# Kernel optimization log

Measured on AMD Instinct MI355X. Metric: run time of the kernel, lower is better.

The kernel has to match this reference:

```python
import jax, jax.numpy as jnp
import numpy as np

BS = 8            # self.b from __init__
NSAMPLE = 32      # self.nsample
EPS_TCR = 0.2     # TotalCodingRate eps
COS_EPS = 1e-8    # torch cosine_similarity eps


def setup_inputs() -> dict:
    key = jax.random.key(0)
    k0, k1, k2, k3, k4 = jax.random.split(key, 5)
    B, N, C = 8, 8192, 64
    return {
        "logits": jax.random.normal(k0, (B, N, C), jnp.float32),
        "logits1": jax.random.normal(k1, (B, N, C), jnp.float32),
        "p0first": jax.random.uniform(k2, (B, N, 3), jnp.float32),
        "p0sec": jax.random.uniform(k3, (B, N, 3), jnp.float32),
        "orixyz": jax.random.uniform(k4, (B, N, 3), jnp.float32),
    }


def _fps(p, m):
    # furthest point sampling, seed = point 0; p: [b,n,3] -> idx [b,m] int32
    b, n, _ = p.shape
    batch = jnp.arange(b)
    d0 = jnp.sum((p - p[:, :1]) ** 2, -1)  # [b,n] sq dist to seed

    def step(dist, _):
        nxt = jnp.argmax(dist, axis=1)                 # [b]
        pn = p[batch, nxt]                             # [b,3]
        dist = jnp.minimum(dist, jnp.sum((p - pn[:, None]) ** 2, -1))
        return dist, nxt

    _, idxs = jax.lax.scan(step, d0, None, length=m - 1)  # [m-1,b]
    return jnp.concatenate(
        [jnp.zeros((b, 1), jnp.int32), idxs.T.astype(jnp.int32)], axis=1)


def _knn_idx(q, s, k):
    # q: [b,m,3] queries, s: [b,n,3] support -> [b,m,k] neighbor indices
    d = (jnp.sum(q * q, -1)[:, :, None] + jnp.sum(s * s, -1)[:, None, :]
         - 2.0 * jnp.einsum('bmd,bnd->bmn', q, s))
    _, idx = jax.lax.top_k(-d, k)  # smallest distances
    return idx


def _group_losses(fi, fj, c):
    # fi: [b,m,c] center feats, fj: [b,m,k,c] neighbor feats
    # per group: datatemp = cat(fj, fi) -> [K=k+1, c]
    D = jnp.concatenate([fj, fi[:, :, None, :]], axis=2)  # [b,m,K,c]
    avg = D.mean(axis=2, keepdims=True)                   # [b,m,1,c]
    num = jnp.sum(D * avg, -1)                            # [b,m,K]
    den = jnp.maximum(
        jnp.linalg.norm(D, axis=-1) * jnp.linalg.norm(avg, axis=-1), COS_EPS)
    loss_contract = -(num / den).mean(axis=2)             # [b,m] (Similarity_Loss)
    # TotalCodingRate on each single row z: -0.5*logdet(I + (c/(BS*eps)) z z^T)
    #   = -0.5*log(1 + (c/(BS*eps)) ||z||^2)   (rank-1 identity)
    scalar = c / (BS * EPS_TCR)
    loss_tcr = (-0.5 * jnp.log1p(scalar * jnp.sum(D * D, -1))).mean(axis=2)
    return jnp.sum(200.0 * loss_contract + 1.0 * loss_tcr, axis=1)  # [b]


def reference(logits, logits1, p0first, p0sec, orixyz):
    b, n, c = logits.shape
    ds = n // 16  # downsample

    # global per-point cosine loss
    num = jnp.sum(logits * logits1, -1)
    den = jnp.maximum(
        jnp.linalg.norm(logits, axis=-1) * jnp.linalg.norm(logits1, axis=-1),
        COS_EPS)
    globalpointloss = -jnp.mean(num / den)

    idx = _fps(p0first, ds)   # [b,ds]
    idx1 = _fps(p0sec, ds)
    new_p = jnp.take_along_axis(p0first, idx[..., None], axis=1)   # [b,ds,3]
    new_p1 = jnp.take_along_axis(p0sec, idx1[..., None], axis=1)
    fi = jnp.take_along_axis(logits, idx[..., None], axis=1)       # [b,ds,c]
    fi1 = jnp.take_along_axis(logits1, idx1[..., None], axis=1)

    ki = _knn_idx(new_p, p0first, NSAMPLE)    # [b,ds,k]
    ki1 = _knn_idx(new_p1, p0sec, NSAMPLE)
    fj = jax.vmap(lambda f, i: f[i])(logits, ki)    # [b,ds,k,c]
    fj1 = jax.vmap(lambda f, i: f[i])(logits1, ki1)

    # per-batch summed group-inner losses (both views)
    S = _group_losses(fi, fj, c) + _group_losses(fi1, fj1, c)  # [b]

    # faithful to original: running total divided by downsample each batch iter
    def fold(g, s):
        return (g + s) / ds, None
    groupinnerloss, _ = jax.lax.scan(fold, jnp.float32(0.0), S)
    groupinnerloss = groupinnerloss / b

    # original returns globalpointloss + groupinnerloss + groupinnerloss
    # (groupouterloss is computed but never used in the returned loss)
    return globalpointloss + groupinnerloss + groupinnerloss
```

## Files before the change

### kernel.cpp

```cpp
#include <hip/hip_runtime.h>
#include <cstdint>

#define NPTS 8192
#define NB 8
#define DS 512
#define CF 64
#define KNN 32
#define NFPS 16
#define NWORK 240
#define NCOSI 64
#define NITEMS (NCOSI + 2 * NB * DS)
#define DYNLDS 98304

typedef float v2f __attribute__((ext_vector_type(2)));
typedef unsigned long long ull;

__device__ __forceinline__ float wave_max63(float x) {
  int v;
  v = __builtin_amdgcn_update_dpp(0, __float_as_int(x), 0x111, 0xf, 0xf, true); x = fmaxf(x, __int_as_float(v));
  v = __builtin_amdgcn_update_dpp(0, __float_as_int(x), 0x112, 0xf, 0xf, true); x = fmaxf(x, __int_as_float(v));
  v = __builtin_amdgcn_update_dpp(0, __float_as_int(x), 0x114, 0xf, 0xf, true); x = fmaxf(x, __int_as_float(v));
  v = __builtin_amdgcn_update_dpp(0, __float_as_int(x), 0x118, 0xf, 0xf, true); x = fmaxf(x, __int_as_float(v));
  v = __builtin_amdgcn_update_dpp(0, __float_as_int(x), 0x142, 0xf, 0xf, true); x = fmaxf(x, __int_as_float(v));
  v = __builtin_amdgcn_update_dpp(0, __float_as_int(x), 0x143, 0xf, 0xf, true); x = fmaxf(x, __int_as_float(v));
  return x;
}

__device__ __forceinline__ float wave_sum_bcast(float x) {
  int v;
  v = __builtin_amdgcn_update_dpp(0, __float_as_int(x), 0x111, 0xf, 0xf, true); x += __int_as_float(v);
  v = __builtin_amdgcn_update_dpp(0, __float_as_int(x), 0x112, 0xf, 0xf, true); x += __int_as_float(v);
  v = __builtin_amdgcn_update_dpp(0, __float_as_int(x), 0x114, 0xf, 0xf, true); x += __int_as_float(v);
  v = __builtin_amdgcn_update_dpp(0, __float_as_int(x), 0x118, 0xf, 0xf, true); x += __int_as_float(v);
  v = __builtin_amdgcn_update_dpp(0, __float_as_int(x), 0x142, 0xf, 0xf, true); x += __int_as_float(v);
  v = __builtin_amdgcn_update_dpp(0, __float_as_int(x), 0x143, 0xf, 0xf, true); x += __int_as_float(v);
  return __int_as_float(__builtin_amdgcn_readlane(__float_as_int(x), 63));
}

__global__ __launch_bounds__(64) void zero_kernel(float* __restrict__ acc) {
  if (threadIdx.x < 16) acc[threadIdx.x] = 0.0f;
}

__global__ __launch_bounds__(512, 2) void fused_kernel(
    const float* __restrict__ logits, const float* __restrict__ logits1,
    const float* __restrict__ p0first, const float* __restrict__ p0sec,
    int* __restrict__ idxbuf, float* __restrict__ acc,
    int* __restrict__ done, float* __restrict__ out) {
  extern __shared__ char smem[];
  __shared__ __align__(16) ull wslot[2][4];
  __shared__ int wtot[8];
  __shared__ int s_bl[2];
  __shared__ int ctr, eqctr, s_center;
  __shared__ float wloss[8];

  const int blk = blockIdx.x;
  const int t = threadIdx.x;

  if (blk < NFPS) {
    float* ldsP = (float*)smem;
    const int view = blk >> 3, b = blk & 7;
    const float* p = (view ? p0sec : p0first) + (size_t)b * NPTS * 3;
    int* idx_out = idxbuf + blk * DS;
    const int lane = t & 63, wave = t >> 6;

    if (t < 256) {
      v2f px2[16], py2[16], pz2[16], dist2[16];
      {
        const float4* p4 = (const float4*)p;
        float4* l4 = (float4*)ldsP;
#pragma unroll
        for (int k = 0; k < 8; ++k) {
          float4 v0 = p4[t * 24 + 3 * k + 0];
          float4 v1 = p4[t * 24 + 3 * k + 1];
          float4 v2 = p4[t * 24 + 3 * k + 2];
          l4[t * 24 + 3 * k + 0] = v0;
          l4[t * 24 + 3 * k + 1] = v1;
          l4[t * 24 + 3 * k + 2] = v2;
          px2[2 * k]     = (v2f){v0.x, v0.w};
          py2[2 * k]     = (v2f){v0.y, v1.x};
          pz2[2 * k]     = (v2f){v0.z, v1.y};
          px2[2 * k + 1] = (v2f){v1.z, v2.y};
          py2[2 * k + 1] = (v2f){v1.w, v2.z};
          pz2[2 * k + 1] = (v2f){v2.x, v2.w};
          dist2[2 * k] = (v2f){3.4e38f, 3.4e38f};
          dist2[2 * k + 1] = (v2f){3.4e38f, 3.4e38f};
        }
      }
#pragma unroll
      for (int g = 0; g < 16; ++g) {
        asm("" : "+v"(px2[g]), "+v"(py2[g]), "+v"(pz2[g]));
      }
      if (t == 0)
        __hip_atomic_store(&idx_out[0], 0, __ATOMIC_RELAXED, __HIP_MEMORY_SCOPE_AGENT);
      float wx = p[0], wy = p[1], wz = p[2];
      __syncthreads();

      for (int it = 0; it < DS - 1; ++it) {
        v2f wx2 = (v2f){wx, wx}, wy2 = (v2f){wy, wy}, wz2 = (v2f){wz, wz};
#pragma unroll
        for (int g = 0; g < 16; ++g) {
          v2f dx = px2[g] - wx2, dy = py2[g] - wy2, dz = pz2[g] - wz2;
          v2f nd = dx * dx + dy * dy + dz * dz;
          dist2[g] = __builtin_elementwise_min(dist2[g], nd);
        }
        v2f m0 = __builtin_elementwise_max(dist2[0], dist2[1]);
        v2f m1 = __builtin_elementwise_max(dist2[2], dist2[3]);
        v2f m2 = __builtin_elementwise_max(dist2[4], dist2[5]);
        v2f m3 = __builtin_elementwise_max(dist2[6], dist2[7]);
        v2f m4 = __builtin_elementwise_max(dist2[8], dist2[9]);
        v2f m5 = __builtin_elementwise_max(dist2[10], dist2[11]);
        v2f m6 = __builtin_elementwise_max(dist2[12], dist2[13]);
        v2f m7 = __builtin_elementwise_max(dist2[14], dist2[15]);
        v2f n0 = __builtin_elementwise_max(m0, m1);
        v2f n1 = __builtin_elementwise_max(m2, m3);
        v2f n2 = __builtin_elementwise_max(m4, m5);
        v2f n3 = __builtin_elementwise_max(m6, m7);
        v2f o0 = __builtin_elementwise_max(n0, n1);
        v2f o1 = __builtin_elementwise_max(n2, n3);
        v2f q = __builtin_elementwise_max(o0, o1);
        float lm = fmaxf(q.x, q.y);
        float wmv = wave_max63(lm);
        float wm = __int_as_float(__builtin_amdgcn_readlane(__float_as_int(wmv), 63));
        ull cmask = __ballot(lm == wm);
        int winlane = (int)__ffsll(cmask) - 1;
        if (lane == winlane) {
          int jbest = 0;
#pragma unroll
          for (int jp = 31; jp >= 0; --jp) {
            float dv = (jp & 1) ? dist2[jp >> 1].y : dist2[jp >> 1].x;
            if (dv == lm) jbest = jp;
          }
          unsigned e_best = ((unsigned)t << 5) | (unsigned)jbest;
          wslot[it & 1][wave] =
              (((ull)__float_as_uint(wm)) << 32) | (ull)(8191u - e_best);
        }
        asm volatile("s_waitcnt lgkmcnt(0)\n\ts_barrier" ::: "memory");
        {
          const ull* ws = wslot[it & 1];
          ull k0 = ws[0], k1 = ws[1], k2 = ws[2], k3 = ws[3];
          ull a0 = k0 > k1 ? k0 : k1, a1 = k2 > k3 ? k2 : k3;
          ull kb = a0 > a1 ? a0 : a1;
          unsigned e = 8191u - (unsigned)(kb & 0xffffffffu);
          if (t == 0)
            __hip_atomic_store(&idx_out[it + 1], (int)e, __ATOMIC_RELAXED,
                               __HIP_MEMORY_SCOPE_AGENT);
          wx = ldsP[e * 3 + 0]; wy = ldsP[e * 3 + 1]; wz = ldsP[e * 3 + 2];
        }
      }
    } else {
      __syncthreads();
      for (int it = 0; it < DS - 1; ++it)
        asm volatile("s_waitcnt lgkmcnt(0)\n\ts_barrier" ::: "memory");
    }
  } else {
    int* hb0 = (int*)smem;
    int* hb1 = (int*)(smem + 16384);
    float* Drows = (float*)(smem + 32768);
    int* nbr = (int*)(smem + 41216);
    int* eq = (int*)(smem + 41344);
    const int lane = t & 63, wave = t >> 6;
    const int w0 = blk - NFPS;
    for (int item = w0; item < NITEMS; item += NWORK) {
      if (item < NCOSI) {
        float cv = 0.0f;
#pragma unroll
        for (int rr = 0; rr < 2; ++rr) {
          int row = item * 1024 + rr * 512 + t;
          const float4* A = (const float4*)(logits + (size_t)row * CF);
          const float4* Bv = (const float4*)(logits1 + (size_t)row * CF);
          float ab = 0.f, aa = 0.f, bb = 0.f;
#pragma unroll
          for (int i = 0; i < 16; ++i) {
            float4 a = A[i], c4 = Bv[i];
            ab += a.x * c4.x + a.y * c4.y + a.z * c4.z + a.w * c4.w;
            aa += a.x * a.x + a.y * a.y + a.z * a.z + a.w * a.w;
            bb += c4.x * c4.x + c4.y * c4.y + c4.z * c4.z + c4.w * c4.w;
          }
          cv += ab / fmaxf(sqrtf(aa) * sqrtf(bb), 1e-8f);
        }
        cv = wave_sum_bcast(cv);
        if (lane == 0) wloss[wave] = cv;
        __syncthreads();
        if (t == 0) {
          float s = 0.f;
#pragma unroll
          for (int w = 0; w < 8; ++w) s += wloss[w];
          atomicAdd(&acc[0], s);
        }
        __syncthreads();
      } else {
        const int qi2 = item - NCOSI;
        const int m = qi2 >> 4, pair = qi2 & 15;
        const int g = pair * DS + m;
        const int view = pair >> 3, b = pair & 7;
        const float* p = (view ? p0sec : p0first) + (size_t)b * NPTS * 3;
        float f48[48];
        {
          const float4* p4 = (const float4*)p;
#pragma unroll
          for (int i = 0; i < 12; ++i) {
            float4 v4 = p4[t * 12 + i];
            f48[i * 4 + 0] = v4.x; f48[i * 4 + 1] = v4.y;
            f48[i * 4 + 2] = v4.z; f48[i * 4 + 3] = v4.w;
          }
        }
        for (int k = t; k < 4096; k += 512) hb0[k] = 0;
        if (t == 0) {
          int ce;
          while ((unsigned)(ce = __hip_atomic_load(&idxbuf[g], __ATOMIC_RELAXED,
                                                   __HIP_MEMORY_SCOPE_AGENT)) >= 8192u)
            __builtin_amdgcn_s_sleep(2);
          s_center = ce;
        }
        __syncthreads();
        const int ci = s_center;
        const float qx = p[ci * 3], qy = p[ci * 3 + 1], qz = p[ci * 3 + 2];
        const float qq = qx * qx + qy * qy + qz * qz;
        const int cpy = (t & 1) << 11;
        unsigned sk[16];
#pragma unroll
        for (int j = 0; j < 16; ++j) {
          float sx = f48[j * 3], sy = f48[j * 3 + 1], sz = f48[j * 3 + 2];
          float ss = sx * sx + sy * sy + sz * sz;
          float dt = qx * sx + qy * sy + qz * sz;
          float d = qq + ss - 2.0f * dt;
          unsigned u = __float_as_uint(d);
          u = (u & 0x80000000u) ? ~u : (u | 0x80000000u);
          sk[j] = u;
        }
        int rrank = 31;
#pragma unroll
        for (int j = 0; j < 16; ++j) atomicAdd(&hb0[cpy + (sk[j] >> 21)], 1);
        __syncthreads();
        unsigned pA, pAB, V;
        {
          int b0 = t << 2;
          int c0 = hb0[b0] + hb0[2048 + b0];
          int c1 = hb0[b0 + 1] + hb0[2048 + b0 + 1];
          int c2 = hb0[b0 + 2] + hb0[2048 + b0 + 2];
          int c3 = hb0[b0 + 3] + hb0[2048 + b0 + 3];
          int s = c0 + c1 + c2 + c3;
          int inc = s;
#pragma unroll
          for (int o = 1; o < 64; o <<= 1) {
            int v = __shfl_up(inc, o, 64);
            if (lane >= o) inc += v;
          }
          if (lane == 63) wtot[wave] = inc;
          for (int k = t; k < 4096; k += 512) hb1[k] = 0;
          __syncthreads();
          int off = 0;
#pragma unroll
          for (int w = 0; w < 8; ++w) off += (w < wave) ? wtot[w] : 0;
          int exc = off + inc - s;
          if (rrank >= exc && rrank < exc + s) {
            int r2 = rrank - exc; int bin, less;
            if (r2 < c0) { bin = 0; less = 0; }
            else if (r2 < c0 + c1) { bin = 1; less = c0; }
            else if (r2 < c0 + c1 + c2) { bin = 2; less = c0 + c1; }
            else { bin = 3; less = c0 + c1 + c2; }
            s_bl[0] = b0 + bin; s_bl[1] = exc + less;
          }
          __syncthreads();
          pA = (unsigned)s_bl[0];
          rrank -= s_bl[1];
        }
#pragma unroll
        for (int j = 0; j < 16; ++j) {
          unsigned u = sk[j];
          if ((u >> 21) == pA) atomicAdd(&hb1[cpy + ((u >> 10) & 2047)], 1);
        }
        __syncthreads();
        {
          int b0 = t << 2;
          int c0 = hb1[b0] + hb1[2048 + b0];
          int c1 = hb1[b0 + 1] + hb1[2048 + b0 + 1];
          int c2 = hb1[b0 + 2] + hb1[2048 + b0 + 2];
          int c3 = hb1[b0 + 3] + hb1[2048 + b0 + 3];
          int s = c0 + c1 + c2 + c3;
          int inc = s;
#pragma unroll
          for (int o = 1; o < 64; o <<= 1) {
            int v = __shfl_up(inc, o, 64);
            if (lane >= o) inc += v;
          }
          if (lane == 63) wtot[wave] = inc;
          for (int k = t; k < 4096; k += 512) hb0[k] = 0;
          __syncthreads();
          int off = 0;
#pragma unroll
          for (int w = 0; w < 8; ++w) off += (w < wave) ? wtot[w] : 0;
          int exc = off + inc - s;
          if (rrank >= exc && rrank < exc + s) {
            int r2 = rrank - exc; int bin, less;
            if (r2 < c0) { bin = 0; less = 0; }
            else if (r2 < c0 + c1) { bin = 1; less = c0; }
            else if (r2 < c0 + c1 + c2) { bin = 2; less = c0 + c1; }
            else { bin = 3; less = c0 + c1 + c2; }
            s_bl[0] = b0 + bin; s_bl[1] = exc + less;
          }
          __syncthreads();
          pAB = (pA << 11) | (unsigned)s_bl[0];
          rrank -= s_bl[1];
        }
        const int cpyC = (t & 1) << 10;
#pragma unroll
        for (int j = 0; j < 16; ++j) {
          unsigned u = sk[j];
          if ((u >> 10) == pAB) atomicAdd(&hb0[cpyC + (u & 1023)], 1);
        }
        __syncthreads();
        {
          int b0 = t << 1;
          int c0 = hb0[b0] + hb0[1024 + b0];
          int c1 = hb0[b0 + 1] + hb0[1024 + b0 + 1];
          int s = c0 + c1;
          int inc = s;
#pragma unroll
          for (int o = 1; o < 64; o <<= 1) {
            int v = __shfl_up(inc, o, 64);
            if (lane >= o) inc += v;
          }
          if (lane == 63) wtot[wave] = inc;
          __syncthreads();
          int off = 0;
#pragma unroll
          for (int w = 0; w < 8; ++w) off += (w < wave) ? wtot[w] : 0;
          int exc = off + inc - s;
          if (rrank >= exc && rrank < exc + s) {
            int r2 = rrank - exc;
            if (r2 < c0) { s_bl[0] = b0; s_bl[1] = exc; }
            else { s_bl[0] = b0 + 1; s_bl[1] = exc + c0; }
          }
          if (t == 0) { ctr = 0; eqctr = 0; }
          __syncthreads();
          V = (pAB << 10) | (unsigned)s_bl[0];
          rrank -= s_bl[1];
        }
#pragma unroll
        for (int j = 0; j < 16; ++j) {
          unsigned u = sk[j];
          if (u < V) {
            int s = atomicAdd(&ctr, 1);
            nbr[s] = t * 16 + j;
          } else if (u == V) {
            int s2 = atomicAdd(&eqctr, 1);
            if (s2 < 256) eq[s2] = t * 16 + j;
          }
        }
        __syncthreads();
        if (t == 0) {
          int need = rrank + 1;
          int E = eqctr; if (E > 256) E = 256;
          int base = KNN - need;
          for (int s = 0; s < need; ++s) {
            int mi = 0;
            for (int i = 1; i < E; ++i)
              if (eq[i] < eq[mi]) mi = i;
            nbr[base + s] = eq[mi];
            eq[mi] = 0x7fffffff;
          }
        }
        __syncthreads();
        const float* f = (view ? logits1 : logits) + (size_t)b * NPTS * CF;
        for (int r = wave; r < 33; r += 8) {
          int e = (r < 32) ? nbr[r] : ci;
          Drows[r * 64 + lane] = f[(size_t)e * CF + lane];
        }
        __syncthreads();
        float avg = 0.0f;
#pragma unroll
        for (int r = 0; r < 33; ++r) avg += Drows[r * 64 + lane];
        avg *= (1.0f / 33.0f);
        float na = wave_sum_bcast(avg * avg);
        const float rsna = sqrtf(na);
        float loss = 0.0f;
        for (int r = wave; r < 33; r += 8) {
          float d = Drows[r * 64 + lane];
          float d0 = wave_sum_bcast(d * avg);
          float n0 = wave_sum_bcast(d * d);
          float den = fmaxf(sqrtf(n0) * rsna, 1e-8f);
          loss += -200.0f * (d0 / den) - 0.5f * log1pf(40.0f * n0);
        }
        if (lane == 0) wloss[wave] = loss;
        __syncthreads();
        if (t == 0) {
          float s = 0.f;
#pragma unroll
          for (int w = 0; w < 8; ++w) s += wloss[w];
          atomicAdd(&acc[1 + b], s * (1.0f / 33.0f));
        }
        __syncthreads();
      }
    }
    __syncthreads();
    if (t == 0) {
      int d = __hip_atomic_fetch_add(done, 1, __ATOMIC_ACQ_REL, __HIP_MEMORY_SCOPE_AGENT);
      if (d == NWORK - 1) {
        float a0 = __hip_atomic_load(&acc[0], __ATOMIC_ACQUIRE, __HIP_MEMORY_SCOPE_AGENT);
        float gsum = 0.0f;
        for (int bb = 0; bb < 8; ++bb) {
          float Sb = __hip_atomic_load(&acc[1 + bb], __ATOMIC_ACQUIRE, __HIP_MEMORY_SCOPE_AGENT);
          gsum = (gsum + Sb) * (1.0f / 512.0f);
        }
        gsum *= 0.125f;
        out[0] = -a0 / 65536.0f + gsum + gsum;
      }
    }
  }
}

extern "C" void kernel_launch(void* const* d_in, const int* in_sizes, int n_in,
                              void* d_out, int out_size, void* d_ws, size_t ws_size,
                              hipStream_t stream) {
  (void)in_sizes; (void)n_in; (void)out_size; (void)ws_size;
  const float* logits  = (const float*)d_in[0];
  const float* logits1 = (const float*)d_in[1];
  const float* p0first = (const float*)d_in[2];
  const float* p0sec   = (const float*)d_in[3];
  float* out = (float*)d_out;

  float* acc = (float*)d_ws;
  int* done  = (int*)d_ws + 13;
  int* idxbuf = (int*)d_ws + 16;

  zero_kernel<<<1, 64, 0, stream>>>(acc);
  fused_kernel<<<NFPS + NWORK, 512, DYNLDS, stream>>>(logits, logits1, p0first, p0sec,
                                                      idxbuf, acc, done, out);
}
```

Before: 542.3 us.

## Pack two FPS instances per block with flag-based wave sync instead of barriers

Each FPS block now runs two independent furthest-point-sampling instances (one per group of 4 waves), halving the FPS block count and giving the freed blocks to the worker pool. The per-iteration s_barrier is replaced by tagged atomic slot stores and spin-polling on LDS, so each group syncs only its own 4 waves. Winner coordinates are read from global memory (L1/L2) instead of an LDS copy. Spin-polling adds LDS traffic and relies on the waves of a group being co-resident and making progress. The global reads sit on the serial critical path of every iteration.

```diff
diff --git a/kernel.cpp b/kernel.cpp
--- a/kernel.cpp
+++ b/kernel.cpp
@@ -6,8 +6,8 @@
 #define DS 512
 #define CF 64
 #define KNN 32
-#define NFPS 16
-#define NWORK 240
+#define NFPS 8
+#define NWORK 248
 #define NCOSI 64
 #define NITEMS (NCOSI + 2 * NB * DS)
 #define DYNLDS 98304
@@ -41,13 +41,14 @@
   if (threadIdx.x < 16) acc[threadIdx.x] = 0.0f;
 }
 
-__global__ __launch_bounds__(512, 2) void fused_kernel(
+__global__ __attribute__((amdgpu_waves_per_eu(2, 2))) __launch_bounds__(512)
+void fused_kernel(
     const float* __restrict__ logits, const float* __restrict__ logits1,
     const float* __restrict__ p0first, const float* __restrict__ p0sec,
     int* __restrict__ idxbuf, float* __restrict__ acc,
     int* __restrict__ done, float* __restrict__ out) {
   extern __shared__ char smem[];
-  __shared__ __align__(16) ull wslot[2][4];
+  __shared__ __align__(16) ull slots[2][2][4];
   __shared__ int wtot[8];
   __shared__ int s_bl[2];
   __shared__ int ctr, eqctr, s_center;
@@ -57,100 +58,105 @@
   const int t = threadIdx.x;
 
   if (blk < NFPS) {
-    float* ldsP = (float*)smem;
-    const int view = blk >> 3, b = blk & 7;
-    const float* p = (view ? p0sec : p0first) + (size_t)b * NPTS * 3;
-    int* idx_out = idxbuf + blk * DS;
     const int lane = t & 63, wave = t >> 6;
-
-    if (t < 256) {
-      v2f px2[16], py2[16], pz2[16], dist2[16];
-      {
-        const float4* p4 = (const float4*)p;
-        float4* l4 = (float4*)ldsP;
-#pragma unroll
-        for (int k = 0; k < 8; ++k) {
-          float4 v0 = p4[t * 24 + 3 * k + 0];
-          float4 v1 = p4[t * 24 + 3 * k + 1];
-          float4 v2 = p4[t * 24 + 3 * k + 2];
-          l4[t * 24 + 3 * k + 0] = v0;
-          l4[t * 24 + 3 * k + 1] = v1;
-          l4[t * 24 + 3 * k + 2] = v2;
-          px2[2 * k]     = (v2f){v0.x, v0.w};
-          py2[2 * k]     = (v2f){v0.y, v1.x};
-          pz2[2 * k]     = (v2f){v0.z, v1.y};
-          px2[2 * k + 1] = (v2f){v1.z, v2.y};
-          py2[2 * k + 1] = (v2f){v1.w, v2.z};
-          pz2[2 * k + 1] = (v2f){v2.x, v2.w};
-          dist2[2 * k] = (v2f){3.4e38f, 3.4e38f};
-          dist2[2 * k + 1] = (v2f){3.4e38f, 3.4e38f};
-        }
-      }
+    const int group = wave >> 2;
+    const int gwave = wave & 3;
+    const int inst = blk * 2 + group;
+    const float* p = ((inst >> 3) ? p0sec : p0first) + (size_t)(inst & 7) * NPTS * 3;
+    int* idx_out = idxbuf + inst * DS;
+    const int lt = (gwave << 6) | lane;
+
+    v2f px2[16], py2[16], pz2[16], dist2[16];
+    {
+      const float4* p4 = (const float4*)p;
+#pragma unroll
+      for (int k = 0; k < 8; ++k) {
+        float4 v0 = p4[lt * 24 + 3 * k + 0];
+        float4 v1 = p4[lt * 24 + 3 * k + 1];
+        float4 v2 = p4[lt * 24 + 3 * k + 2];
+        px2[2 * k]     = (v2f){v0.x, v0.w};
+        py2[2 * k]     = (v2f){v0.y, v1.x};
+        pz2[2 * k]     = (v2f){v0.z, v1.y};
+        px2[2 * k + 1] = (v2f){v1.z, v2.y};
+        py2[2 * k + 1] = (v2f){v1.w, v2.z};
+        pz2[2 * k + 1] = (v2f){v2.x, v2.w};
+        dist2[2 * k] = (v2f){3.4e38f, 3.4e38f};
+        dist2[2 * k + 1] = (v2f){3.4e38f, 3.4e38f};
+      }
+    }
+    if (t < 16) ((ull*)slots)[t] = 0ull;
+    if (lt == 0)
+      __hip_atomic_store(&idx_out[0], 0, __ATOMIC_RELAXED, __HIP_MEMORY_SCOPE_AGENT);
+    float wx = p[0], wy = p[1], wz = p[2];
+    __syncthreads();
+
+    for (int it = 0; it < DS - 1; ++it) {
 #pragma unroll
       for (int g = 0; g < 16; ++g) {
-        asm("" : "+v"(px2[g]), "+v"(py2[g]), "+v"(pz2[g]));
-      }
-      if (t == 0)
-        __hip_atomic_store(&idx_out[0], 0, __ATOMIC_RELAXED, __HIP_MEMORY_SCOPE_AGENT);
-      float wx = p[0], wy = p[1], wz = p[2];
-      __syncthreads();
-
-      for (int it = 0; it < DS - 1; ++it) {
-        v2f wx2 = (v2f){wx, wx}, wy2 = (v2f){wy, wy}, wz2 = (v2f){wz, wz};
-#pragma unroll
-        for (int g = 0; g < 16; ++g) {
-          v2f dx = px2[g] - wx2, dy = py2[g] - wy2, dz = pz2[g] - wz2;
-          v2f nd = dx * dx + dy * dy + dz * dz;
-          dist2[g] = __builtin_elementwise_min(dist2[g], nd);
-        }
-        v2f m0 = __builtin_elementwise_max(dist2[0], dist2[1]);
-        v2f m1 = __builtin_elementwise_max(dist2[2], dist2[3]);
-        v2f m2 = __builtin_elementwise_max(dist2[4], dist2[5]);
-        v2f m3 = __builtin_elementwise_max(dist2[6], dist2[7]);
-        v2f m4 = __builtin_elementwise_max(dist2[8], dist2[9]);
-        v2f m5 = __builtin_elementwise_max(dist2[10], dist2[11]);
-        v2f m6 = __builtin_elementwise_max(dist2[12], dist2[13]);
-        v2f m7 = __builtin_elementwise_max(dist2[14], dist2[15]);
-        v2f n0 = __builtin_elementwise_max(m0, m1);
-        v2f n1 = __builtin_elementwise_max(m2, m3);
-        v2f n2 = __builtin_elementwise_max(m4, m5);
-        v2f n3 = __builtin_elementwise_max(m6, m7);
-        v2f o0 = __builtin_elementwise_max(n0, n1);
-        v2f o1 = __builtin_elementwise_max(n2, n3);
-        v2f q = __builtin_elementwise_max(o0, o1);
-        float lm = fmaxf(q.x, q.y);
-        float wmv = wave_max63(lm);
-        float wm = __int_as_float(__builtin_amdgcn_readlane(__float_as_int(wmv), 63));
-        ull cmask = __ballot(lm == wm);
-        int winlane = (int)__ffsll(cmask) - 1;
-        if (lane == winlane) {
-          int jbest = 0;
-#pragma unroll
-          for (int jp = 31; jp >= 0; --jp) {
-            float dv = (jp & 1) ? dist2[jp >> 1].y : dist2[jp >> 1].x;
-            if (dv == lm) jbest = jp;
-          }
-          unsigned e_best = ((unsigned)t << 5) | (unsigned)jbest;
-          wslot[it & 1][wave] =
-              (((ull)__float_as_uint(wm)) << 32) | (ull)(8191u - e_best);
-        }
-        asm volatile("s_waitcnt lgkmcnt(0)\n\ts_barrier" ::: "memory");
-        {
-          const ull* ws = wslot[it & 1];
-          ull k0 = ws[0], k1 = ws[1], k2 = ws[2], k3 = ws[3];
-          ull a0 = k0 > k1 ? k0 : k1, a1 = k2 > k3 ? k2 : k3;
-          ull kb = a0 > a1 ? a0 : a1;
-          unsigned e = 8191u - (unsigned)(kb & 0xffffffffu);
-          if (t == 0)
-            __hip_atomic_store(&idx_out[it + 1], (int)e, __ATOMIC_RELAXED,
-                               __HIP_MEMORY_SCOPE_AGENT);
-          wx = ldsP[e * 3 + 0]; wy = ldsP[e * 3 + 1]; wz = ldsP[e * 3 + 2];
-        }
-      }
-    } else {
-      __syncthreads();
-      for (int it = 0; it < DS - 1; ++it)
-        asm volatile("s_waitcnt lgkmcnt(0)\n\ts_barrier" ::: "memory");
+        asm("" : "+v"(px2[g]), "+v"(py2[g]), "+v"(pz2[g]), "+v"(dist2[g]));
+      }
+      v2f wx2 = (v2f){wx, wx}, wy2 = (v2f){wy, wy}, wz2 = (v2f){wz, wz};
+#pragma unroll
+      for (int g = 0; g < 16; ++g) {
+        v2f dx = px2[g] - wx2, dy = py2[g] - wy2, dz = pz2[g] - wz2;
+        v2f nd = dx * dx + dy * dy + dz * dz;
+        dist2[g] = __builtin_elementwise_min(dist2[g], nd);
+      }
+      v2f m0 = __builtin_elementwise_max(dist2[0], dist2[1]);
+      v2f m1 = __builtin_elementwise_max(dist2[2], dist2[3]);
+      v2f m2 = __builtin_elementwise_max(dist2[4], dist2[5]);
+      v2f m3 = __builtin_elementwise_max(dist2[6], dist2[7]);
+      v2f m4 = __builtin_elementwise_max(dist2[8], dist2[9]);
+      v2f m5 = __builtin_elementwise_max(dist2[10], dist2[11]);
+      v2f m6 = __builtin_elementwise_max(dist2[12], dist2[13]);
+      v2f m7 = __builtin_elementwise_max(dist2[14], dist2[15]);
+      v2f n0 = __builtin_elementwise_max(m0, m1);
+      v2f n1 = __builtin_elementwise_max(m2, m3);
+      v2f n2 = __builtin_elementwise_max(m4, m5);
+      v2f n3 = __builtin_elementwise_max(m6, m7);
+      v2f o0 = __builtin_elementwise_max(n0, n1);
+      v2f o1 = __builtin_elementwise_max(n2, n3);
+      v2f q = __builtin_elementwise_max(o0, o1);
+      float lm = fmaxf(q.x, q.y);
+      float wmv = wave_max63(lm);
+      float wm = __int_as_float(__builtin_amdgcn_readlane(__float_as_int(wmv), 63));
+      ull cmask = __ballot(lm == wm);
+      int winlane = (int)__ffsll(cmask) - 1;
+      if (lane == winlane) {
+        int jbest = 0;
+#pragma unroll
+        for (int jp = 31; jp >= 0; --jp) {
+          float dv = (jp & 1) ? dist2[jp >> 1].y : dist2[jp >> 1].x;
+          if (dv == lm) jbest = jp;
+        }
+        unsigned e_best = ((unsigned)lt << 5) | (unsigned)jbest;
+        ull key = (((ull)__float_as_uint(wm)) << 32) |
+                  (((ull)(unsigned)(it + 1)) << 13) | (ull)(8191u - e_best);
+        __hip_atomic_store(&slots[it & 1][group][gwave], key, __ATOMIC_RELAXED,
+                           __HIP_MEMORY_SCOPE_WORKGROUP);
+      }
+      const unsigned want = (unsigned)(it + 1);
+      ull k0, k1, k2, k3;
+      for (;;) {
+        k0 = __hip_atomic_load(&slots[it & 1][group][0], __ATOMIC_RELAXED,
+                               __HIP_MEMORY_SCOPE_WORKGROUP);
+        k1 = __hip_atomic_load(&slots[it & 1][group][1], __ATOMIC_RELAXED,
+                               __HIP_MEMORY_SCOPE_WORKGROUP);
+        k2 = __hip_atomic_load(&slots[it & 1][group][2], __ATOMIC_RELAXED,
+                               __HIP_MEMORY_SCOPE_WORKGROUP);
+        k3 = __hip_atomic_load(&slots[it & 1][group][3], __ATOMIC_RELAXED,
+                               __HIP_MEMORY_SCOPE_WORKGROUP);
+        if ((((unsigned)k0 >> 13) == want) & (((unsigned)k1 >> 13) == want) &
+            (((unsigned)k2 >> 13) == want) & (((unsigned)k3 >> 13) == want))
+          break;
+      }
+      ull a0 = k0 > k1 ? k0 : k1, a1 = k2 > k3 ? k2 : k3;
+      ull kb = a0 > a1 ? a0 : a1;
+      unsigned e = 8191u - (unsigned)(kb & 0x1fffu);
+      if (lt == 0)
+        __hip_atomic_store(&idx_out[it + 1], (int)e, __ATOMIC_RELAXED,
+                           __HIP_MEMORY_SCOPE_AGENT);
+      wx = p[e * 3 + 0]; wy = p[e * 3 + 1]; wz = p[e * 3 + 2];
     }
   } else {
     int* hb0 = (int*)smem;
```

After: 946.6 us. +74.6%, slower.
